# Performance work log

Measured on AMD Instinct MI355X. Metric: run time of the kernel, lower is better.

## Reference

```python
import jax, jax.numpy as jnp
import numpy as np

SHIFT = 1  # fixed shift_direction (module draws +/-1 at random; we pin +1)

def setup_inputs() -> dict:
    key = jax.random.key(0)
    kx, kw = jax.random.split(key)
    x = jax.random.normal(kx, (1024, 256, 7, 7), dtype=jnp.float32)
    W = jax.random.normal(kw, (128, 3, 3, 512), dtype=jnp.float32)
    return {"x": x, "W": W}

def _fwd(x, W):
    B = x.shape[0]
    t = x.reshape(B, 256, 7, 7)
    # unfold((3,1), padding=(1,0)) along H: t[b,c,k,h,w] = x_pad[b,c,h+k-1,w]
    xp = jnp.pad(t, ((0, 0), (0, 0), (1, 1), (0, 0)))
    t = jnp.stack([xp[:, :, k:k + 7, :] for k in range(3)], axis=2)  # (B,256,3,7,7)
    t = t.reshape(B, 2, 128, 3, 7, 7).transpose(0, 2, 3, 4, 1, 5)   # (B,128,3,7,2,7)
    t = t.reshape(B, 128, 3, 14, 7)
    t = jnp.roll(t, SHIFT, axis=3)
    t = t.reshape(B, 128, 3, 7, 2, 7).sum(axis=4)                   # (B,128,3,7,7)
    t = t.transpose(0, 1, 3, 2, 4)                                  # (B,128,7,3,7)
    t = jnp.roll(t, SHIFT, axis=4)
    # second unfold((3,1), padding=(1,0)) along W dim: gather 3 shifted slices
    tp = jnp.pad(t, ((0, 0), (0, 0), (0, 0), (0, 0), (1, 1)))
    t3 = jnp.stack([tp[..., k2:k2 + 7] for k2 in range(3)], axis=-1)  # (B,128,7,3,7,3) = (m,l,n,j,o,k)
    out = jnp.einsum('mlnjok,ljki->mnoi', t3, W)                     # (B,7,7,512)
    return out.transpose(0, 3, 1, 2)                                 # (B,512,7,7)

def reference(x, W):
    return _fwd(x, W)
```

## Files before the change

kernel.cpp:

```cpp
#include <hip/hip_runtime.h>

typedef __attribute__((ext_vector_type(8)))  __bf16 bvec8;
typedef __attribute__((ext_vector_type(4)))  __bf16 bvec4;
typedef __attribute__((ext_vector_type(16))) float  fvec16;
typedef __attribute__((ext_vector_type(8)))  short  svec8;

__global__ __launch_bounds__(256) void pack_w(const float* __restrict__ W,
                                              __bf16* __restrict__ Wp) {
    int u = blockIdx.x * 256 + threadIdx.x;
    if (u >= 73728) return;
    int lane = u & 63;
    int h    = (u >> 6) & 1;
    int it   = (u >> 7) & 15;
    int t    = u >> 11;
    int i  = (it << 5) + (lane & 31);
    int K0 = ((2 * t + h) << 4) + ((lane >> 5) << 3);
    bvec8 o;
#pragma unroll
    for (int e = 0; e < 8; ++e) {
        int K  = K0 + e;
        int jk = K >> 7;
        int l  = K & 127;
        int j  = (jk * 11) >> 5;
        int k  = jk - 3 * j;
        o[e] = (__bf16)W[((l * 9 + j * 3 + k) << 9) + i];
    }
    *(bvec8*)&Wp[(size_t)u * 8] = o;
}

__global__ __launch_bounds__(1024, 4) void conv_mfma(
    const float* __restrict__ x, const __bf16* __restrict__ Wp,
    float* __restrict__ out)
{
    __shared__ __align__(16) char smem[65024];
    __bf16* xs = (__bf16*)smem;
    __bf16* ys = (__bf16*)(smem + 25088);

    const int tid  = threadIdx.x;
    const int lane = tid & 63;
    const int l31  = lane & 31;
    const int ls5  = lane >> 5;
    const int wd   = tid >> 6;
    const int b0   = blockIdx.x * 2;

    const float* xb  = x + (size_t)b0 * 12544;
    const char*  WpB = (const char*)Wp;
    const int wbase  = wd * 2048 + lane * 16;

    bvec8 aE[2], aO[2];
#pragma unroll
    for (int h = 0; h < 2; ++h) {
        aE[h] = *(const bvec8*)(WpB + wbase + (h << 10));
        aO[h] = *(const bvec8*)(WpB + 32768 + wbase + (h << 10));
    }

    for (int bb = 0; bb < 2; ++bb) {
        for (int it = 0; it < 4; ++it) {
            int e4 = it * 1024 + tid;
            if (e4 < 3136) {
                const float4 v = ((const float4*)(xb + bb * 12544))[e4];
                bvec4 pk = { (__bf16)v.x, (__bf16)v.y, (__bf16)v.z, (__bf16)v.w };
                *(bvec4*)&xs[e4 * 4] = pk;
            }
        }
        __syncthreads();
        for (int it = 0; it < 2; ++it) {
            int up = it * 1024 + tid;
            if (up < 1248) {
                int row  = up >> 4;
                int useg = up & 15;
                int l0   = useg * 8;
                bvec8 ov;
                if (row == 77) {
                    ov = __builtin_bit_cast(bvec8, (svec8)0);
                } else if (row < 63) {
                    int t = row / 7, w = row - t * 7;
                    int tb = t + 5; if (tb >= 7) tb -= 7;
                    int cB = tb * 7 + w;
                    bool mA = (t >= 1) && (t <= 7);
                    int cA = mA ? (t - 1) * 7 + w : 0;
#pragma unroll
                    for (int d = 0; d < 8; ++d) {
                        float fa = mA ? (float)xs[(l0 + d) * 49 + cA] : 0.f;
                        float fb = (float)xs[(128 + l0 + d) * 49 + cB];
                        ov[d] = (__bf16)(fa + fb);
                    }
                } else if (row < 70) {
                    int w = row - 63;
#pragma unroll
                    for (int d = 0; d < 8; ++d) ov[d] = xs[(l0 + d) * 49 + w];
                } else {
                    int w = row - 70;
#pragma unroll
                    for (int d = 0; d < 8; ++d) ov[d] = xs[(l0 + d) * 49 + 7 + w];
                }
                *(bvec8*)&ys[((bb * 78 + row) << 7) + ((useg ^ (row & 15)) << 3)] = ov;
            }
        }
        __syncthreads();
    }

    int nq[2], oo[2];
#pragma unroll
    for (int sn = 0; sn < 2; ++sn) {
        int s = sn * 32 + l31;
        int sc = (s < 49) ? s : 48;
        nq[sn] = sc / 7;
        oo[sn] = sc - nq[sn] * 7;
    }

    fvec16 acc[2][2];
#pragma unroll
    for (int sn = 0; sn < 2; ++sn)
#pragma unroll
        for (int bb = 0; bb < 2; ++bb)
#pragma unroll
            for (int r = 0; r < 16; ++r) acc[sn][bb][r] = 0.f;

#define GEO(JK, ROWE, RX) {                                                   \
        int j_ = ((JK) * 11) >> 5; int k_ = (JK) - 3 * j_;                    \
        _Pragma("unroll")                                                     \
        for (int sn_ = 0; sn_ < 2; ++sn_) {                                   \
            int tw_ = oo[sn_] + k_ + 5; int w_ = tw_ >= 7 ? tw_ - 7 : tw_;    \
            int row_ = (nq[sn_] + j_) * 7 + w_;                               \
            if (nq[sn_] == 1 && j_ == 0) row_ = 63 + w_;                      \
            if (nq[sn_] == 0 && j_ == 2) row_ = 70 + w_;                      \
            if ((k_ == 0 && oo[sn_] == 0) || (k_ == 2 && oo[sn_] == 6))       \
                row_ = 77;                                                    \
            ROWE[sn_] = row_ << 7; RX[sn_] = row_ & 15; } }

#define STEP(P, AW, TNEXT, DOPF) {                                            \
        bvec8 bf[2][2];                                                       \
        __builtin_amdgcn_s_setprio(1);                                        \
        _Pragma("unroll")                                                     \
        for (int h_ = 0; h_ < 2; ++h_) {                                      \
            _Pragma("unroll")                                                 \
            for (int sn_ = 0; sn_ < 2; ++sn_) {                               \
                int u_ = ((P) * 4 + h_ * 2 + ls5) ^ rx[sn_];                  \
                bf[sn_][0] = *(const bvec8*)&ys[rowE[sn_] + (u_ << 3)];       \
                bf[sn_][1] = *(const bvec8*)&ys[9984 + rowE[sn_] + (u_ << 3)];\
            }                                                                 \
            _Pragma("unroll")                                                 \
            for (int sn_ = 0; sn_ < 2; ++sn_)                                 \
            _Pragma("unroll")                                                 \
            for (int bb_ = 0; bb_ < 2; ++bb_)                                 \
                acc[sn_][bb_] = __builtin_amdgcn_mfma_f32_32x32x16_bf16(      \
                    AW[h_], bf[sn_][bb_], acc[sn_][bb_], 0, 0, 0);            \
        }                                                                     \
        __builtin_amdgcn_s_setprio(0);                                        \
        if (DOPF) {                                                           \
            const char* gp_ = WpB + ((size_t)(TNEXT) << 15) + wbase;          \
            AW[0] = *(const bvec8*)(gp_);                                     \
            AW[1] = *(const bvec8*)(gp_ + 1024);                              \
        } }

    int rowE[2], rx[2];
    for (int jk = 0; jk < 9; ++jk) {
        const int t0 = jk * 4;
        GEO(jk, rowE, rx);
        STEP(0, aE, t0 + 2, true)
        STEP(1, aO, t0 + 3, true)
        STEP(2, aE, t0 + 4, (jk < 8))
        STEP(3, aO, t0 + 5, (jk < 8))
    }

#undef GEO
#undef STEP

    const int i0 = wd * 32 + 4 * ls5;
#pragma unroll
    for (int sn = 0; sn < 2; ++sn) {
        if (sn == 1 && l31 >= 17) continue;
        const int s = sn * 32 + l31;
#pragma unroll
        for (int bb = 0; bb < 2; ++bb) {
            const size_t ob = (size_t)(b0 + bb) * 25088;
#pragma unroll
            for (int r = 0; r < 16; ++r) {
                int i = i0 + (r & 3) + 8 * (r >> 2);
                out[ob + (size_t)i * 49 + s] = acc[sn][bb][r];
            }
        }
    }
}

extern "C" void kernel_launch(void* const* d_in, const int* in_sizes, int n_in,
                              void* d_out, int out_size, void* d_ws, size_t ws_size,
                              hipStream_t stream) {
    const float* x = (const float*)d_in[0];
    const float* W = (const float*)d_in[1];
    float* out = (float*)d_out;
    __bf16* Wp = (__bf16*)d_ws;
    (void)in_sizes; (void)n_in; (void)out_size; (void)ws_size;

    hipLaunchKernelGGL(pack_w, dim3(288), dim3(256), 0, stream, W, Wp);
    hipLaunchKernelGGL(conv_mfma, dim3(512), dim3(1024), 0, stream, x, Wp, out);
}
```

Before: 90.08 us.

## Remap warps so each covers two M-tiles for one batch item

Each of the 16 warps previously computed a 32-row output tile for both batch items sharing one weight fragment. Now 8 warps per batch item each compute two 32-row M-tiles, reusing one LDS B-fragment across two MFMAs and loading twice the weight data per step. This halves per-warp LDS reads but doubles global/L2 weight fetches per warp and changes the prefetch schedule to one step ahead instead of two.

```diff
diff --git a/kernel.cpp b/kernel.cpp
--- a/kernel.cpp
+++ b/kernel.cpp
@@ -41,18 +41,21 @@
     const int l31  = lane & 31;
     const int ls5  = lane >> 5;
     const int wd   = tid >> 6;
+    const int wi   = wd & 7;
+    const int bbw  = wd >> 3;
     const int b0   = blockIdx.x * 2;
 
     const float* xb  = x + (size_t)b0 * 12544;
     const char*  WpB = (const char*)Wp;
-    const int wbase  = wd * 2048 + lane * 16;
+    const int wbase  = wi * 4096 + lane * 16;
+    const int ysb    = bbw * 9984;
 
-    bvec8 aE[2], aO[2];
+    bvec8 aW[2][2];
 #pragma unroll
-    for (int h = 0; h < 2; ++h) {
-        aE[h] = *(const bvec8*)(WpB + wbase + (h << 10));
-        aO[h] = *(const bvec8*)(WpB + 32768 + wbase + (h << 10));
-    }
+    for (int am = 0; am < 2; ++am)
+#pragma unroll
+        for (int h = 0; h < 2; ++h)
+            aW[am][h] = *(const bvec8*)(WpB + wbase + am * 2048 + h * 1024);
 
     for (int bb = 0; bb < 2; ++bb) {
         for (int it = 0; it < 4; ++it) {
@@ -111,13 +114,13 @@
 
     fvec16 acc[2][2];
 #pragma unroll
-    for (int sn = 0; sn < 2; ++sn)
+    for (int am = 0; am < 2; ++am)
 #pragma unroll
-        for (int bb = 0; bb < 2; ++bb)
+        for (int sn = 0; sn < 2; ++sn)
 #pragma unroll
-            for (int r = 0; r < 16; ++r) acc[sn][bb][r] = 0.f;
+            for (int r = 0; r < 16; ++r) acc[am][sn][r] = 0.f;
 
-#define GEO(JK, ROWE, RX) {                                                   \
+#define GEO(JK) {                                                             \
         int j_ = ((JK) * 11) >> 5; int k_ = (JK) - 3 * j_;                    \
         _Pragma("unroll")                                                     \
         for (int sn_ = 0; sn_ < 2; ++sn_) {                                   \
@@ -127,58 +130,56 @@
             if (nq[sn_] == 0 && j_ == 2) row_ = 70 + w_;                      \
             if ((k_ == 0 && oo[sn_] == 0) || (k_ == 2 && oo[sn_] == 6))       \
                 row_ = 77;                                                    \
-            ROWE[sn_] = row_ << 7; RX[sn_] = row_ & 15; } }
+            rowE[sn_] = ysb + ((row_) << 7); rx[sn_] = row_ & 15; } }
 
-#define STEP(P, AW, TNEXT, DOPF) {                                            \
-        bvec8 bf[2][2];                                                       \
+#define STEP(P, TNEXT, DOPF) {                                                \
         __builtin_amdgcn_s_setprio(1);                                        \
         _Pragma("unroll")                                                     \
-        for (int h_ = 0; h_ < 2; ++h_) {                                      \
+        for (int h_ = 0; h_ < 2; ++h_)                                        \
+        _Pragma("unroll")                                                     \
+        for (int sn_ = 0; sn_ < 2; ++sn_) {                                   \
+            int u_ = ((P) * 4 + h_ * 2 + ls5) ^ rx[sn_];                      \
+            bvec8 bf_ = *(const bvec8*)&ys[rowE[sn_] + (u_ << 3)];            \
             _Pragma("unroll")                                                 \
-            for (int sn_ = 0; sn_ < 2; ++sn_) {                               \
-                int u_ = ((P) * 4 + h_ * 2 + ls5) ^ rx[sn_];                  \
-                bf[sn_][0] = *(const bvec8*)&ys[rowE[sn_] + (u_ << 3)];       \
-                bf[sn_][1] = *(const bvec8*)&ys[9984 + rowE[sn_] + (u_ << 3)];\
-            }                                                                 \
-            _Pragma("unroll")                                                 \
-            for (int sn_ = 0; sn_ < 2; ++sn_)                                 \
-            _Pragma("unroll")                                                 \
-            for (int bb_ = 0; bb_ < 2; ++bb_)                                 \
-                acc[sn_][bb_] = __builtin_amdgcn_mfma_f32_32x32x16_bf16(      \
-                    AW[h_], bf[sn_][bb_], acc[sn_][bb_], 0, 0, 0);            \
+            for (int am_ = 0; am_ < 2; ++am_)                                 \
+                acc[am_][sn_] = __builtin_amdgcn_mfma_f32_32x32x16_bf16(      \
+                    aW[am_][h_], bf_, acc[am_][sn_], 0, 0, 0);                \
         }                                                                     \
         __builtin_amdgcn_s_setprio(0);                                        \
         if (DOPF) {                                                           \
             const char* gp_ = WpB + ((size_t)(TNEXT) << 15) + wbase;          \
-            AW[0] = *(const bvec8*)(gp_);                                     \
-            AW[1] = *(const bvec8*)(gp_ + 1024);                              \
+            _Pragma("unroll")                                                 \
+            for (int am_ = 0; am_ < 2; ++am_)                                 \
+            _Pragma("unroll")                                                 \
+            for (int h_ = 0; h_ < 2; ++h_)                                    \
+                aW[am_][h_] = *(const bvec8*)(gp_ + am_ * 2048 + h_ * 1024);  \
         } }
 
     int rowE[2], rx[2];
     for (int jk = 0; jk < 9; ++jk) {
         const int t0 = jk * 4;
-        GEO(jk, rowE, rx);
-        STEP(0, aE, t0 + 2, true)
-        STEP(1, aO, t0 + 3, true)
-        STEP(2, aE, t0 + 4, (jk < 8))
-        STEP(3, aO, t0 + 5, (jk < 8))
+        GEO(jk);
+        STEP(0, t0 + 1, true)
+        STEP(1, t0 + 2, true)
+        STEP(2, t0 + 3, true)
+        STEP(3, t0 + 4, (jk < 8))
     }
 
 #undef GEO
 #undef STEP
 
-    const int i0 = wd * 32 + 4 * ls5;
+    const size_t ob = (size_t)(b0 + bbw) * 25088;
 #pragma unroll
-    for (int sn = 0; sn < 2; ++sn) {
-        if (sn == 1 && l31 >= 17) continue;
-        const int s = sn * 32 + l31;
+    for (int am = 0; am < 2; ++am) {
+        const int i0 = wi * 64 + am * 32 + 4 * ls5;
 #pragma unroll
-        for (int bb = 0; bb < 2; ++bb) {
-            const size_t ob = (size_t)(b0 + bb) * 25088;
+        for (int sn = 0; sn < 2; ++sn) {
+            if (sn == 1 && l31 >= 17) continue;
+            const int s = sn * 32 + l31;
 #pragma unroll
             for (int r = 0; r < 16; ++r) {
                 int i = i0 + (r & 3) + 8 * (r >> 2);
-                out[ob + (size_t)i * 49 + s] = acc[sn][bb][r];
+                out[ob + (size_t)i * 49 + s] = acc[am][sn][r];
             }
         }
     }
```

Result: slower. 96.76 us (+7.4%).
